# Kernel optimization log

Hardware: AMD Instinct MI355X
Metric: run time of the kernel (lower is better)

## Reference

```python
import jax, jax.numpy as jnp
import numpy as np

N_E = 512; KEY_DIM = 512; E_DIM = 512; E_SPLIT = 8
KT = 0.1; COE_EMA = 0.5; RATE = 1.2
HALF_PI = float(np.pi / 2.0)


def l2n(x, eps=1e-12):
    # torch F.normalize(p=2, dim=-1)
    return x / jnp.maximum(jnp.linalg.norm(x, axis=-1, keepdims=True), eps)


def sphere_emb(feature, t):
    # TimeSphereEncoder: lift unit feature in R^d to R^{d+1} with time angle
    # a = t * (pi/2) / rate ; out = [feature*cos(a), sin(a)]
    a = t * (HALF_PI / RATE)
    return jnp.concatenate([feature * jnp.cos(a)[..., None], jnp.sin(a)[..., None]], axis=-1)


def split_t_f(x):
    # inverse of sphere_emb for unit-norm x: recover (t, sin_component, feature)
    s = x[..., -1]
    t = jnp.arcsin(jnp.clip(s, -1.0, 1.0)) / (HALF_PI / RATE)
    f = l2n(x[..., :-1])
    return t, s, f


def split_norm(v):
    # split_vparams_norm: L2-normalize each of E_SPLIT contiguous chunks
    shp = v.shape
    d = E_DIM // E_SPLIT
    return l2n(v.reshape(shp[:-1] + (E_SPLIT, d))).reshape(shp)


def setup_inputs() -> dict:
    key = jax.random.key(0)
    k = jax.random.split(key, 6)
    key_soft = jax.random.normal(k[0], (32, 1024, KEY_DIM), jnp.float32)
    u_t = jax.random.uniform(k[1], (32, 1024), jnp.float32)
    keys_weight = l2n(jax.random.uniform(k[2], (N_E, KEY_DIM), jnp.float32, -1.0 / N_E, 1.0 / N_E))
    t_keys_weight = (jnp.arange(N_E, dtype=jnp.float32)[:, None]
                     + jax.random.uniform(k[3], (N_E, 1), jnp.float32)) / N_E
    r_keys_weight = jnp.full((N_E, 1), 0.999, jnp.float32)
    vparams_weight = jax.random.uniform(k[4], (N_E, E_DIM), jnp.float32, -1.0 / N_E, 1.0 / N_E)
    return {"key_soft": key_soft, "u_t": u_t, "keys_weight": keys_weight,
            "t_keys_weight": t_keys_weight, "r_keys_weight": r_keys_weight,
            "vparams_weight": vparams_weight}


def _forward(key_soft, u_t, keys_weight, t_keys_weight, r_keys_weight, vparams_weight):
    sg = jax.lax.stop_gradient
    B, T, D = key_soft.shape
    BT = B * T
    # normalize + time-embed tokens
    ks_emb = sphere_emb(l2n(key_soft), u_t)                       # (B,T,D+1)
    ks_flat = ks_emb.reshape(BT, D + 1)
    # codebook keys: normalized, time-embedded, detached, scaled by hardtanh(r)
    keys_norm = sphere_emb(l2n(keys_weight), t_keys_weight[:, 0])  # (n_e,D+1)
    r = jnp.clip(r_keys_weight, 0.0, 1.0)                          # (n_e,1)
    keysA = sg(keys_norm) * r
    score0 = ks_flat @ keysA.T                                     # (BT,n_e)
    idx0 = jnp.argmax(score0, axis=1)
    # --- EMA codebook update (all no-grad) ---
    ks_sg = sg(ks_flat)
    seg = jax.ops.segment_sum(ks_sg, idx0, num_segments=N_E)       # (n_e,D+1)
    cnt = jax.ops.segment_sum(jnp.ones((BT,), ks_sg.dtype), idx0, num_segments=N_E)[:, None]
    mean_ks = jnp.nan_to_num(seg / (1.0 + cnt))
    keys_new_full = l2n(sg(keysA) * COE_EMA + mean_ks * (1.0 - COE_EMA))
    t_new, _, feat_new = split_t_f(keys_new_full)
    index_switch = jnp.argsort(t_new)
    t_sorted = t_new[index_switch]
    keys_feat2 = feat_new[index_switch]
    r2 = jnp.clip(r_keys_weight[index_switch], 0.0, 1.0)
    vparams2 = vparams_weight[index_switch]
    idx1 = index_switch[idx0]
    cnt2 = jax.ops.segment_sum(jnp.ones((BT,), ks_sg.dtype), idx1, num_segments=N_E) + 1.0
    w_cnt = sg(jnp.nan_to_num(1.0 / cnt2)[idx1].reshape(B, T))
    # --- second scoring with updated codebook ---
    keys_norm2 = sphere_emb(l2n(keys_feat2), t_sorted)             # (n_e,D+1)
    keysB = sg(keys_norm2) * r2
    score = ks_flat @ keysB.T                                      # (BT,n_e)
    w = jnp.nan_to_num(jax.nn.softmax(score / KT, axis=-1))
    w_max = jnp.take_along_axis(w, idx1[:, None], axis=-1)[:, 0].reshape(B, T)
    vpn = split_norm(vparams2)
    vp_w = split_norm(w @ sg(vpn))                                 # (BT,e_dim)
    key_w = l2n(w @ sg(keysB))                                     # (BT,D+1)
    vparams_hard = split_norm(vparams2[idx1])
    key_hard_raw = keysB[idx1]
    vparams_hard = vp_w + sg(vparams_hard - vp_w)                  # straight-through
    key_hard = key_w + sg(key_hard_raw - key_w)
    return (idx1.reshape(B, T),
            key_hard.reshape(B, T, D + 1),
            vp_w.reshape(B, T, E_DIM),
            vparams_hard.reshape(B, T, E_DIM),
            w_max, w_cnt, ks_emb)


def reference(key_soft, u_t, keys_weight, t_keys_weight, r_keys_weight, vparams_weight):
    return _forward(key_soft, u_t, keys_weight, t_keys_weight, r_keys_weight, vparams_weight)
```

## Files before the change

### kernel.cpp

```cpp
#include <hip/hip_runtime.h>
#include <math.h>

constexpr int BT  = 32768;
constexpr int D   = 512;
constexpr int D1  = 513;
constexpr int NE  = 512;
constexpr int EDIM = 512;
constexpr int NCH = 128;
constexpr int SUB = 16;
constexpr int P1S = 520;
constexpr int AKP = 544;
#define KA 1.3089969389957472f

typedef _Float16 h16;
typedef _Float16 f16x8 __attribute__((ext_vector_type(8)));
typedef _Float16 f16x4 __attribute__((ext_vector_type(4)));
typedef float f32x4 __attribute__((ext_vector_type(4)));

__device__ __forceinline__ float wave_sum(float v) {
#pragma unroll
  for (int off = 32; off; off >>= 1) v += __shfl_xor(v, off);
  return v;
}

__global__ __launch_bounds__(256) void k_embed(const float* __restrict__ ks,
                                               const float* __restrict__ ut,
                                               float* __restrict__ emb) {
  int token = blockIdx.x * 4 + (threadIdx.x >> 6);
  int lane = threadIdx.x & 63;
  const float4* row4 = (const float4*)(ks + (size_t)token * D);
  float4 va = row4[lane * 2];
  float4 vb = row4[lane * 2 + 1];
  float ss = va.x * va.x + va.y * va.y + va.z * va.z + va.w * va.w
           + vb.x * vb.x + vb.y * vb.y + vb.z * vb.z + vb.w * vb.w;
  ss = wave_sum(ss);
  float inv = 1.0f / fmaxf(sqrtf(ss), 1e-12f);
  float a = ut[token] * KA;
  float c = cosf(a), s = sinf(a);
  float ic = inv * c;
  float* o = emb + (size_t)token * D1 + lane * 8;
  o[0] = va.x * ic; o[1] = va.y * ic; o[2] = va.z * ic; o[3] = va.w * ic;
  o[4] = vb.x * ic; o[5] = vb.y * ic; o[6] = vb.z * ic; o[7] = vb.w * ic;
  if (lane == 0) emb[(size_t)token * D1 + D] = s;
}

__global__ __launch_bounds__(64) void k_keysA(const float* __restrict__ kw,
                                              const float* __restrict__ tk,
                                              const float* __restrict__ rk,
                                              float* __restrict__ keysA) {
  int e = blockIdx.x; int lane = threadIdx.x;
  const float* row = kw + (size_t)e * D;
  float v[8]; float ss = 0.f;
#pragma unroll
  for (int i = 0; i < 8; i++) { v[i] = row[lane + 64 * i]; ss += v[i] * v[i]; }
  ss = wave_sum(ss);
  float inv = 1.0f / fmaxf(sqrtf(ss), 1e-12f);
  float a = tk[e] * KA;
  float r = fminf(fmaxf(rk[e], 0.f), 1.f);
  float c = cosf(a) * r, s = sinf(a) * r;
  float* o = keysA + (size_t)e * D1;
#pragma unroll
  for (int i = 0; i < 8; i++) o[lane + 64 * i] = v[i] * inv * c;
  if (lane == 0) o[D] = s;
}

__global__ __launch_bounds__(64) void k_split2(const float* __restrict__ in,
                                               h16* __restrict__ out,
                                               int ncol, int kp) {
  int e = blockIdx.x; int lane = threadIdx.x;
  const float* r = in + (size_t)e * ncol;
  h16* o = out + (size_t)e * 2 * kp;
  for (int c = lane; c < kp; c += 64) {
    float x = (c < ncol) ? r[c] * 8.0f : 0.f;
    h16 h = (h16)x;
    o[c] = h;
    o[kp + c] = (h16)(x - (float)h);
  }
}

template <int KP, int EPI, int ASRC, int TERMS>
__global__ __launch_bounds__(256) void k_gemm3(const float* __restrict__ Af,
                                               const h16* __restrict__ Ai,
                                               const h16* __restrict__ Bp,
                                               float* __restrict__ C,
                                               unsigned short* __restrict__ W,
                                               float* __restrict__ pv,
                                               int* __restrict__ pi_,
                                               float* __restrict__ ps) {
  constexpr int NS = KP / 32;
  constexpr int LST = 36;
  __shared__ h16 Ah[128 * LST];
  __shared__ h16 Al[(TERMS >= 2) ? 128 * LST : 1];
  __shared__ h16 Bh[128 * LST];
  __shared__ h16 Bl[(TERMS >= 3) ? 128 * LST : 1];
  const int tid = threadIdx.x;
  const int bid = blockIdx.x;
  const int wg = (bid & 7) * (gridDim.x >> 3) + (bid >> 3);
  const int m0 = (wg >> 2) * 128;
  const int n0 = (wg & 3) * 128;
  const int nblk = wg & 3;
  const int lane = tid & 63;
  const int wid = tid >> 6;
  const int wr = wid >> 1, wc = wid & 1;
  const int l15 = lane & 15, l4 = lane >> 4;
  const int aB = (wr * 64 + l15) * LST + l4 * 8;
  const int bB = (wc * 64 + l15) * LST + l4 * 8;

  f32x4 acc[4][4] = {};

  auto loadAf = [&](int s, float fv[4][4]) {
    int k0 = s * 32;
    bool guard = (KP == AKP) && (k0 + 32 > D1);
#pragma unroll
    for (int p = 0; p < 4; ++p) {
      int row = (tid >> 3) + 32 * p;
      int fq = tid & 7;
      const float* ap = Af + (size_t)(m0 + row) * D1 + k0 + fq * 4;
      if (!guard) {
#pragma unroll
        for (int j = 0; j < 4; ++j) fv[p][j] = ap[j];
      } else {
#pragma unroll
        for (int j = 0; j < 4; ++j) {
          int c = k0 + fq * 4 + j;
          fv[p][j] = (c < D1) ? ap[j] : 0.f;
        }
      }
    }
  };
  auto writeAf = [&](float fv[4][4]) {
#pragma unroll
    for (int p = 0; p < 4; ++p) {
      int row = (tid >> 3) + 32 * p;
      int fq = tid & 7;
      f16x4 hh, ll;
#pragma unroll
      for (int j = 0; j < 4; ++j) {
        float x = fv[p][j] * 8.0f;
        h16 h = (h16)x;
        hh[j] = h;
        ll[j] = (h16)(x - (float)h);
      }
      *(f16x4*)&Ah[row * LST + fq * 4] = hh;
      if constexpr (TERMS >= 2) *(f16x4*)&Al[row * LST + fq * 4] = ll;
    }
  };
  auto loadAi = [&](int s, uint4 av[2]) {
    int k0 = s * 32;
#pragma unroll
    for (int p = 0; p < 2; ++p) {
      int lin = tid + 256 * p;
      int row = lin >> 2, q = lin & 3;
      av[p] = *(const uint4*)(Ai + (size_t)(m0 + row) * 512 + k0 + q * 8);
    }
  };
  auto writeAi = [&](uint4 av[2]) {
#pragma unroll
    for (int p = 0; p < 2; ++p) {
      int lin = tid + 256 * p;
      int row = lin >> 2, q = lin & 3;
      *(uint4*)&Ah[row * LST + q * 8] = av[p];
    }
  };
  constexpr int BPASS = (TERMS >= 3) ? 4 : 2;
  auto loadB = [&](int s, uint4 bv[BPASS]) {
    int k0 = s * 32;
#pragma unroll
    for (int p = 0; p < BPASS; ++p) {
      int lin = tid + 256 * p;
      int row = (lin >> 2) & 127;
      int half = lin >> 9;
      int q = lin & 3;
      bv[p] = *(const uint4*)(Bp + (size_t)(n0 + row) * (2 * KP) + half * KP + k0 + q * 8);
    }
  };
  auto writeB = [&](uint4 bv[BPASS]) {
#pragma unroll
    for (int p = 0; p < BPASS; ++p) {
      int lin = tid + 256 * p;
      int row = (lin >> 2) & 127;
      int half = lin >> 9;
      int q = lin & 3;
      h16* dst = (half && TERMS >= 3) ? Bl : Bh;
      *(uint4*)&dst[row * LST + q * 8] = bv[p];
    }
  };

  {
    uint4 bv[BPASS];
    loadB(0, bv);
    if constexpr (ASRC == 0) { float fv[4][4]; loadAf(0, fv); writeAf(fv); }
    else { uint4 av[2]; loadAi(0, av); writeAi(av); }
    writeB(bv);
  }
  __syncthreads();

  for (int s = 0; s < NS; ++s) {
    uint4 avn[2], bvn[BPASS]; float fvn[4][4];
    if (s + 1 < NS) {
      if constexpr (ASRC == 0) loadAf(s + 1, fvn);
      else loadAi(s + 1, avn);
      loadB(s + 1, bvn);
    }
    f16x8 ah[4], al_[4];
#pragma unroll
    for (int i = 0; i < 4; ++i) {
      ah[i] = *(const f16x8*)&Ah[aB + i * 16 * LST];
      if constexpr (TERMS >= 2) al_[i] = *(const f16x8*)&Al[aB + i * 16 * LST];
    }
#pragma unroll
    for (int j = 0; j < 4; ++j) {
      f16x8 bh_ = *(const f16x8*)&Bh[bB + j * 16 * LST];
      f16x8 bl_;
      if constexpr (TERMS >= 3) bl_ = *(const f16x8*)&Bl[bB + j * 16 * LST];
#pragma unroll
      for (int i = 0; i < 4; ++i) {
        acc[i][j] = __builtin_amdgcn_mfma_f32_16x16x32_f16(ah[i], bh_, acc[i][j], 0, 0, 0);
        if constexpr (TERMS >= 2)
          acc[i][j] = __builtin_amdgcn_mfma_f32_16x16x32_f16(al_[i], bh_, acc[i][j], 0, 0, 0);
        if constexpr (TERMS >= 3)
          acc[i][j] = __builtin_amdgcn_mfma_f32_16x16x32_f16(ah[i], bl_, acc[i][j], 0, 0, 0);
      }
    }
    __syncthreads();
    if (s + 1 < NS) {
      if constexpr (ASRC == 0) writeAf(fvn);
      else writeAi(avn);
      writeB(bvn);
    }
    __syncthreads();
  }

  if constexpr (EPI == 1) {
#pragma unroll
    for (int i = 0; i < 4; ++i)
#pragma unroll
      for (int r = 0; r < 4; ++r) {
        float ss = 0.f;
#pragma unroll
        for (int j = 0; j < 4; ++j) ss += acc[i][j][r] * acc[i][j][r];
        ss += __shfl_xor(ss, 1); ss += __shfl_xor(ss, 2);
        ss += __shfl_xor(ss, 4); ss += __shfl_xor(ss, 8);
        float inv = 1.0f / fmaxf(sqrtf(ss), 1e-12f);
        int row = m0 + wr * 64 + i * 16 + l4 * 4 + r;
        float* cp = C + (size_t)row * 512 + n0 + wc * 64 + l15;
#pragma unroll
        for (int j = 0; j < 4; ++j) cp[j * 16] = acc[i][j][r] * inv;
      }
  } else if constexpr (EPI == 2) {
    float* lv = (float*)Ah;
    int*   li = (int*)Bh;
#pragma unroll
    for (int i = 0; i < 4; ++i)
#pragma unroll
      for (int r = 0; r < 4; ++r) {
        float bv = -INFINITY; int bidx = 0x7fffffff;
#pragma unroll
        for (int j = 0; j < 4; ++j) {
          float val = acc[i][j][r] * 0.015625f;
          int col = n0 + wc * 64 + j * 16 + l15;
          if (val > bv || (val == bv && col < bidx)) { bv = val; bidx = col; }
        }
#pragma unroll
        for (int off = 1; off < 16; off <<= 1) {
          float ov = __shfl_xor(bv, off);
          int oi = __shfl_xor(bidx, off);
          if (ov > bv || (ov == bv && oi < bidx)) { bv = ov; bidx = oi; }
        }
        if (l15 == 0) {
          int lr = wr * 64 + i * 16 + l4 * 4 + r;
          lv[wc * 128 + lr] = bv; li[wc * 128 + lr] = bidx;
        }
      }
    __syncthreads();
    if (tid < 128) {
      float v0 = lv[tid], v1 = lv[128 + tid];
      int i0 = li[tid], i1 = li[128 + tid];
      bool sec = (v1 > v0) || (v1 == v0 && i1 < i0);
      int row = m0 + tid;
      pv[(size_t)row * 4 + nblk] = sec ? v1 : v0;
      pi_[(size_t)row * 4 + nblk] = sec ? i1 : i0;
    }
  } else if constexpr (EPI == 3) {
    float* psW = (float*)Bh;
#pragma unroll
    for (int i = 0; i < 4; ++i)
#pragma unroll
      for (int r = 0; r < 4; ++r) {
        int row = m0 + wr * 64 + i * 16 + l4 * 4 + r;
        unsigned short* wp = W + (size_t)row * 512 + n0 + wc * 64 + l15;
        float se = 0.f;
#pragma unroll
        for (int j = 0; j < 4; ++j) {
          float v = acc[i][j][r] * 0.015625f;
          float w = __expf(10.f * v);
          se += w;
          h16 hh = (h16)w;
          wp[j * 16] = *(unsigned short*)&hh;
        }
        se += __shfl_xor(se, 1); se += __shfl_xor(se, 2);
        se += __shfl_xor(se, 4); se += __shfl_xor(se, 8);
        if (l15 == 0) psW[wc * 128 + wr * 64 + i * 16 + l4 * 4 + r] = se;
      }
    __syncthreads();
    if (tid < 128)
      ps[(size_t)(m0 + tid) * 4 + nblk] = psW[tid] + psW[128 + tid];
  }
}

__global__ __launch_bounds__(256) void k_argmax_fin(const float* __restrict__ pval,
                                                    const int* __restrict__ pidx,
                                                    int* __restrict__ idx0) {
  int t = blockIdx.x * 256 + threadIdx.x;
  float bv = pval[(size_t)t * 4];
  int bi = pidx[(size_t)t * 4];
#pragma unroll
  for (int b = 1; b < 4; ++b) {
    float v = pval[(size_t)t * 4 + b];
    if (v > bv) { bv = v; bi = pidx[(size_t)t * 4 + b]; }
  }
  idx0[t] = bi;
}

__global__ __launch_bounds__(256) void k_smfin(const float* __restrict__ ps,
                                               const unsigned short* __restrict__ W,
                                               const int* __restrict__ idx1,
                                               float* __restrict__ O4) {
  int t = blockIdx.x * 256 + threadIdx.x;
  float S = ps[(size_t)t * 4] + ps[(size_t)t * 4 + 1]
          + ps[(size_t)t * 4 + 2] + ps[(size_t)t * 4 + 3];
  unsigned short u = W[(size_t)t * 512 + idx1[t]];
  float wsel = (float)(*(const h16*)&u);
  O4[t] = wsel / S;
}

__global__ __launch_bounds__(256) void k_hist_chunks(const int* __restrict__ idx0,
                                                     int* __restrict__ hist2,
                                                     int* __restrict__ myrank) {
  __shared__ int lidx[256];
  __shared__ int hist[NE];
  int tid = threadIdx.x;
  int chunk = blockIdx.x;
  int t = chunk * 256 + tid;
  lidx[tid] = idx0[t];
  hist[tid] = 0; hist[tid + 256] = 0;
  __syncthreads();
  int j = lidx[tid];
  int rank = 0;
  for (int i = 0; i < tid; ++i) rank += (lidx[i] == j);
  myrank[t] = rank;
  atomicAdd(&hist[j], 1);
  __syncthreads();
  hist2[chunk * NE + tid] = hist[tid];
  hist2[chunk * NE + tid + 256] = hist[tid + 256];
}

__global__ __launch_bounds__(512) void k_scan(const int* __restrict__ hist2,
                                              int* __restrict__ offs,
                                              int* __restrict__ chunk_base,
                                              float* __restrict__ cntf) {
  __shared__ int sh[NE];
  int c = threadIdx.x;
  int tot = 0;
  for (int k = 0; k < NCH; ++k) tot += hist2[k * NE + c];
  cntf[c] = (float)tot;
  sh[c] = tot;
  __syncthreads();
  for (int off = 1; off < NE; off <<= 1) {
    int v = (c >= off) ? sh[c - off] : 0;
    __syncthreads();
    sh[c] += v;
    __syncthreads();
  }
  int excl = sh[c] - tot;
  offs[c] = excl;
  int run = excl;
  for (int k = 0; k < NCH; ++k) {
    chunk_base[k * NE + c] = run;
    run += hist2[k * NE + c];
  }
}

__global__ __launch_bounds__(256) void k_scatter(const int* __restrict__ idx0,
                                                 const int* __restrict__ myrank,
                                                 const int* __restrict__ chunk_base,
                                                 int* __restrict__ tok_sorted) {
  int tid = threadIdx.x;
  int chunk = blockIdx.x;
  int t = chunk * 256 + tid;
  int j = idx0[t];
  tok_sorted[chunk_base[chunk * NE + j] + myrank[t]] = t;
}

__global__ __launch_bounds__(256) void k_seg1(const int* __restrict__ tok_sorted,
                                              const int* __restrict__ offs,
                                              const float* __restrict__ cntf,
                                              const float* __restrict__ emb,
                                              float* __restrict__ part1) {
  __shared__ float part[4][512];
  __shared__ float p512[4];
  int e = blockIdx.x, sub = blockIdx.y;
  int tid = threadIdx.x;
  int wave = tid >> 6, lane = tid & 63;
  int start = offs[e];
  int n = (int)cntf[e];
  float acc[8] = {}; float a512 = 0.f;
  for (int k = sub * 4 + wave; k < n; k += SUB * 4) {
    int t = tok_sorted[start + k];
    const float* row = emb + (size_t)t * D1;
#pragma unroll
    for (int i = 0; i < 8; ++i) acc[i] += row[lane + 64 * i];
    if (lane == 0) a512 += row[512];
  }
#pragma unroll
  for (int i = 0; i < 8; ++i) part[wave][lane + 64 * i] = acc[i];
  if (lane == 0) p512[wave] = a512;
  __syncthreads();
  float* o = part1 + (size_t)(e * SUB + sub) * P1S;
  o[tid] = part[0][tid] + part[1][tid] + part[2][tid] + part[3][tid];
  o[tid + 256] = part[0][tid + 256] + part[1][tid + 256] + part[2][tid + 256] + part[3][tid + 256];
  if (tid == 0) o[512] = p512[0] + p512[1] + p512[2] + p512[3];
}

__global__ __launch_bounds__(256) void k_seg2(const float* __restrict__ part1,
                                              const float* __restrict__ cntf,
                                              const float* __restrict__ keysA,
                                              float* __restrict__ feat,
                                              float* __restrict__ tnew) {
  __shared__ float r4[4];
  __shared__ float r4b[4];
  int e = blockIdx.x;
  int tid = threadIdx.x;
  int wave = tid >> 6, lane = tid & 63;
  float s0 = 0.f, s1 = 0.f, s512 = 0.f;
  for (int sub = 0; sub < SUB; ++sub) {
    const float* p = part1 + (size_t)(e * SUB + sub) * P1S;
    s0 += p[tid]; s1 += p[tid + 256]; s512 += p[512];
  }
  float c = cntf[e];
  float rinv = 1.0f / (1.0f + c);
  float x0 = keysA[(size_t)e * D1 + tid] * 0.5f + (s0 * rinv) * 0.5f;
  float x1 = keysA[(size_t)e * D1 + tid + 256] * 0.5f + (s1 * rinv) * 0.5f;
  float x512 = keysA[(size_t)e * D1 + 512] * 0.5f + (s512 * rinv) * 0.5f;
  float ssp = x0 * x0 + x1 * x1;
  float w = wave_sum(ssp);
  if (lane == 0) r4[wave] = w;
  __syncthreads();
  float ss = r4[0] + r4[1] + r4[2] + r4[3] + x512 * x512;
  float inv = 1.0f / fmaxf(sqrtf(ss), 1e-12f);
  if (tid == 0) {
    float sc = fminf(fmaxf(x512 * inv, -1.0f), 1.0f);
    tnew[e] = asinf(sc) / KA;
  }
  float f0 = x0 * inv, f1 = x1 * inv;
  float ssp2 = f0 * f0 + f1 * f1;
  float w2 = wave_sum(ssp2);
  if (lane == 0) r4b[wave] = w2;
  __syncthreads();
  float ss2 = r4b[0] + r4b[1] + r4b[2] + r4b[3];
  float inv2 = 1.0f / fmaxf(sqrtf(ss2), 1e-12f);
  feat[(size_t)e * D + tid] = f0 * inv2;
  feat[(size_t)e * D + tid + 256] = f1 * inv2;
}

__global__ __launch_bounds__(512) void k_argsort(const float* __restrict__ tnew,
                                                 int* __restrict__ perm) {
  __shared__ float t[NE];
  int i = threadIdx.x;
  t[i] = tnew[i];
  __syncthreads();
  float ti = t[i];
  int rank = 0;
  for (int j = 0; j < NE; j++) {
    float tj = t[j];
    rank += (tj < ti) || (tj == ti && j < i);
  }
  perm[rank] = i;
}

__global__ __launch_bounds__(64) void k_build(const int* __restrict__ perm,
                                              const float* __restrict__ tnew,
                                              const float* __restrict__ rk,
                                              const float* __restrict__ feat,
                                              const float* __restrict__ vparams,
                                              float* __restrict__ keysB,
                                              float* __restrict__ vpn,
                                              h16* __restrict__ BV) {
  int p = blockIdx.x; int lane = threadIdx.x;
  int src = perm[p];
  float t = tnew[src];
  float a = t * KA;
  float r2 = fminf(fmaxf(rk[src], 0.f), 1.f);
  float f[8]; float ss = 0.f;
#pragma unroll
  for (int i = 0; i < 8; i++) { f[i] = feat[(size_t)src * D + lane + 64 * i]; ss += f[i] * f[i]; }
  ss = wave_sum(ss);
  float inv = 1.0f / fmaxf(sqrtf(ss), 1e-12f);
  float c = cosf(a) * r2, s = sinf(a) * r2;
#pragma unroll
  for (int i = 0; i < 8; i++) keysB[(size_t)p * D1 + lane + 64 * i] = f[i] * inv * c;
  if (lane == 0) keysB[(size_t)p * D1 + D] = s;
#pragma unroll
  for (int i = 0; i < 8; i++) {
    float vp = vparams[(size_t)src * EDIM + lane + 64 * i];
    float ssc = wave_sum(vp * vp);
    float invc = 1.0f / fmaxf(sqrtf(ssc), 1e-12f);
    float val = vp * invc;
    int d = lane + 64 * i;
    vpn[(size_t)p * EDIM + d] = val;
    float x = val * 8.0f;
    h16 hi = (h16)x;
    BV[(size_t)d * (2 * NE) + p] = hi;
    BV[(size_t)d * (2 * NE) + NE + p] = (h16)(x - (float)hi);
  }
}

__global__ __launch_bounds__(256) void k_idx1(const int* __restrict__ idx0,
                                              const int* __restrict__ perm,
                                              int* __restrict__ idx1,
                                              float* __restrict__ O0) {
  int t = blockIdx.x * 256 + threadIdx.x;
  int j = perm[idx0[t]];
  idx1[t] = j;
  O0[t] = (float)j;
}

__global__ __launch_bounds__(256) void k_gather(const int* __restrict__ idx1,
                                                const int* __restrict__ perm,
                                                const float* __restrict__ cntf,
                                                const float* __restrict__ keysB,
                                                const float* __restrict__ vpn,
                                                float* __restrict__ O1,
                                                float* __restrict__ O3,
                                                float* __restrict__ O5) {
  int t = blockIdx.x * 4 + (threadIdx.x >> 6);
  int lane = threadIdx.x & 63;
  int j = idx1[t];
#pragma unroll
  for (int i = 0; i < 9; i++) {
    int d = lane + 64 * i;
    if (d < D1) O1[(size_t)t * D1 + d] = keysB[(size_t)j * D1 + d];
  }
#pragma unroll
  for (int i = 0; i < 8; i++) {
    int d = lane + 64 * i;
    O3[(size_t)t * EDIM + d] = vpn[(size_t)j * EDIM + d];
  }
  if (lane == 0) O5[t] = 1.0f / (cntf[perm[j]] + 1.0f);
}

extern "C" void kernel_launch(void* const* d_in, const int* in_sizes, int n_in,
                              void* d_out, int out_size, void* d_ws, size_t ws_size,
                              hipStream_t stream) {
  const float* key_soft = (const float*)d_in[0];
  const float* u_t      = (const float*)d_in[1];
  const float* keys_w   = (const float*)d_in[2];
  const float* t_keys   = (const float*)d_in[3];
  const float* r_keys   = (const float*)d_in[4];
  const float* vparams  = (const float*)d_in[5];

  float* out = (float*)d_out;
  float* O0 = out;
  float* O1 = O0 + (size_t)BT;
  float* O2 = O1 + (size_t)BT * D1;
  float* O3 = O2 + (size_t)BT * EDIM;
  float* O4 = O3 + (size_t)BT * EDIM;
  float* O5 = O4 + (size_t)BT;
  float* O6 = O5 + (size_t)BT;

  float* ws = (float*)d_ws;
  size_t off = 0;
  auto alloc = [&](size_t n) { float* p = ws + off; off += (n + 63) & ~(size_t)63; return p; };
  unsigned short* w16 = (unsigned short*)alloc((size_t)BT * 256);
  float* part1  = alloc((size_t)NE * SUB * P1S);
  float* keysA  = alloc((size_t)NE * D1);
  float* keysB  = alloc((size_t)NE * D1);
  float* feat   = alloc((size_t)NE * D);
  float* vpn    = alloc((size_t)NE * EDIM);
  float* tnew   = alloc(NE);
  float* cntf   = alloc(NE);
  h16*   BA     = (h16*)alloc((size_t)NE * AKP);
  h16*   BB     = (h16*)alloc((size_t)NE * AKP);
  h16*   BV     = (h16*)alloc((size_t)EDIM * NE);
  float* pval   = alloc((size_t)BT * 4);
  int*   pidx   = (int*)alloc((size_t)BT * 4);
  float* ps2    = alloc((size_t)BT * 4);
  int*   idx0   = (int*)alloc(BT);
  int*   idx1   = (int*)alloc(BT);
  int*   perm   = (int*)alloc(NE);
  int*   myrank = (int*)alloc(BT);
  int*   tok_sorted = (int*)alloc(BT);
  int*   hist2  = (int*)alloc((size_t)NCH * NE);
  int*   chunk_base = (int*)alloc((size_t)NCH * NE);
  int*   offsb  = (int*)alloc(NE);

  k_embed<<<BT / 4, 256, 0, stream>>>(key_soft, u_t, O6);
  k_keysA<<<NE, 64, 0, stream>>>(keys_w, t_keys, r_keys, keysA);
  k_split2<<<NE, 64, 0, stream>>>(keysA, BA, D1, AKP);
  k_gemm3<AKP, 2, 0, 3><<<1024, 256, 0, stream>>>(O6, nullptr, BA,
                                                  nullptr, nullptr, pval, pidx, nullptr);
  k_argmax_fin<<<BT / 256, 256, 0, stream>>>(pval, pidx, idx0);
  k_hist_chunks<<<NCH, 256, 0, stream>>>(idx0, hist2, myrank);
  k_scan<<<1, NE, 0, stream>>>(hist2, offsb, chunk_base, cntf);
  k_scatter<<<NCH, 256, 0, stream>>>(idx0, myrank, chunk_base, tok_sorted);
  k_seg1<<<dim3(NE, SUB), 256, 0, stream>>>(tok_sorted, offsb, cntf, O6, part1);
  k_seg2<<<NE, 256, 0, stream>>>(part1, cntf, keysA, feat, tnew);
  k_argsort<<<1, NE, 0, stream>>>(tnew, perm);
  k_build<<<NE, 64, 0, stream>>>(perm, tnew, r_keys, feat, vparams, keysB, vpn, BV);
  k_split2<<<NE, 64, 0, stream>>>(keysB, BB, D1, AKP);
  k_idx1<<<BT / 256, 256, 0, stream>>>(idx0, perm, idx1, O0);
  k_gemm3<AKP, 3, 0, 2><<<1024, 256, 0, stream>>>(O6, nullptr, BB,
                                                  nullptr, w16, nullptr, nullptr, ps2);
  k_smfin<<<BT / 256, 256, 0, stream>>>(ps2, w16, idx1, O4);
  k_gemm3<512, 1, 2, 1><<<1024, 256, 0, stream>>>(nullptr, (const h16*)w16, BV,
                                                  O2, nullptr, nullptr, nullptr, nullptr);
  k_gather<<<BT / 4, 256, 0, stream>>>(idx1, perm, cntf, keysB, vpn, O1, O3, O5);
}
```

Before: 443.8 us.

## Precompute fp16 hi/lo split of token embeddings once and fuse small kernels

The embed kernel now also writes a padded fp16 hi/lo split of each token embedding. Both scoring GEMMs load this pre-split A directly instead of re-reading fp32 and splitting it in every tile. The codebook split is folded into k_keysA and k_build, and the argmax-finalize and idx1 kernels are merged into neighbouring kernels, which removes several launches. The cost is an extra 32768x1088 fp16 buffer written once and read twice, and k_seg1 now runs with SUB raised to 32.

```diff
diff --git a/kernel.cpp b/kernel.cpp
--- a/kernel.cpp
+++ b/kernel.cpp
@@ -7,9 +7,10 @@
 constexpr int NE  = 512;
 constexpr int EDIM = 512;
 constexpr int NCH = 128;
-constexpr int SUB = 16;
+constexpr int SUB = 32;
 constexpr int P1S = 520;
 constexpr int AKP = 544;
+constexpr int A16S = 2 * AKP;
 #define KA 1.3089969389957472f
 
 typedef _Float16 h16;
@@ -23,9 +24,20 @@
   return v;
 }
 
+__device__ __forceinline__ void split8(const float* v, float scale, f16x8& hh, f16x8& ll) {
+#pragma unroll
+  for (int j = 0; j < 8; ++j) {
+    float x = v[j] * scale;
+    h16 h = (h16)x;
+    hh[j] = h;
+    ll[j] = (h16)(x - (float)h);
+  }
+}
+
 __global__ __launch_bounds__(256) void k_embed(const float* __restrict__ ks,
                                                const float* __restrict__ ut,
-                                               float* __restrict__ emb) {
+                                               float* __restrict__ emb,
+                                               h16* __restrict__ A16) {
   int token = blockIdx.x * 4 + (threadIdx.x >> 6);
   int lane = threadIdx.x & 63;
   const float4* row4 = (const float4*)(ks + (size_t)token * D);
@@ -38,16 +50,35 @@
   float a = ut[token] * KA;
   float c = cosf(a), s = sinf(a);
   float ic = inv * c;
+  float vals[8] = {va.x * ic, va.y * ic, va.z * ic, va.w * ic,
+                   vb.x * ic, vb.y * ic, vb.z * ic, vb.w * ic};
   float* o = emb + (size_t)token * D1 + lane * 8;
-  o[0] = va.x * ic; o[1] = va.y * ic; o[2] = va.z * ic; o[3] = va.w * ic;
-  o[4] = vb.x * ic; o[5] = vb.y * ic; o[6] = vb.z * ic; o[7] = vb.w * ic;
-  if (lane == 0) emb[(size_t)token * D1 + D] = s;
+#pragma unroll
+  for (int j = 0; j < 8; ++j) o[j] = vals[j];
+  h16* ar = A16 + (size_t)token * A16S;
+  f16x8 hh, ll;
+  split8(vals, 8.0f, hh, ll);
+  *(f16x8*)&ar[lane * 8] = hh;
+  *(f16x8*)&ar[AKP + lane * 8] = ll;
+  if (lane < 4) {
+    f16x8 th = {}, tl = {};
+    if (lane == 0) {
+      emb[(size_t)token * D1 + D] = s;
+      float x = s * 8.0f;
+      h16 h = (h16)x;
+      th[0] = h;
+      tl[0] = (h16)(x - (float)h);
+    }
+    *(f16x8*)&ar[512 + lane * 8] = th;
+    *(f16x8*)&ar[AKP + 512 + lane * 8] = tl;
+  }
 }
 
 __global__ __launch_bounds__(64) void k_keysA(const float* __restrict__ kw,
                                               const float* __restrict__ tk,
                                               const float* __restrict__ rk,
-                                              float* __restrict__ keysA) {
+                                              float* __restrict__ keysA,
+                                              h16* __restrict__ BA) {
   int e = blockIdx.x; int lane = threadIdx.x;
   const float* row = kw + (size_t)e * D;
   float v[8]; float ss = 0.f;
@@ -59,28 +90,31 @@
   float r = fminf(fmaxf(rk[e], 0.f), 1.f);
   float c = cosf(a) * r, s = sinf(a) * r;
   float* o = keysA + (size_t)e * D1;
-#pragma unroll
-  for (int i = 0; i < 8; i++) o[lane + 64 * i] = v[i] * inv * c;
-  if (lane == 0) o[D] = s;
-}
-
-__global__ __launch_bounds__(64) void k_split2(const float* __restrict__ in,
-                                               h16* __restrict__ out,
-                                               int ncol, int kp) {
-  int e = blockIdx.x; int lane = threadIdx.x;
-  const float* r = in + (size_t)e * ncol;
-  h16* o = out + (size_t)e * 2 * kp;
-  for (int c = lane; c < kp; c += 64) {
-    float x = (c < ncol) ? r[c] * 8.0f : 0.f;
+  h16* br = BA + (size_t)e * A16S;
+#pragma unroll
+  for (int i = 0; i < 8; i++) {
+    float val = v[i] * inv * c;
+    o[lane + 64 * i] = val;
+    float x = val * 8.0f;
     h16 h = (h16)x;
-    o[c] = h;
-    o[kp + c] = (h16)(x - (float)h);
+    br[lane + 64 * i] = h;
+    br[AKP + lane + 64 * i] = (h16)(x - (float)h);
+  }
+  if (lane == 0) {
+    o[D] = s;
+    float x = s * 8.0f;
+    h16 h = (h16)x;
+    br[512] = h;
+    br[AKP + 512] = (h16)(x - (float)h);
+  }
+  if (lane >= 1 && lane < 32) {
+    br[512 + lane] = (h16)0.f;
+    br[AKP + 512 + lane] = (h16)0.f;
   }
 }
 
 template <int KP, int EPI, int ASRC, int TERMS>
-__global__ __launch_bounds__(256) void k_gemm3(const float* __restrict__ Af,
-                                               const h16* __restrict__ Ai,
+__global__ __launch_bounds__(256) void k_gemm4(const h16* __restrict__ Ai,
                                                const h16* __restrict__ Bp,
                                                float* __restrict__ C,
                                                unsigned short* __restrict__ W,
@@ -108,44 +142,29 @@
 
   f32x4 acc[4][4] = {};
 
-  auto loadAf = [&](int s, float fv[4][4]) {
+  auto loadA16 = [&](int s, uint4 av[4]) {
     int k0 = s * 32;
-    bool guard = (KP == AKP) && (k0 + 32 > D1);
 #pragma unroll
     for (int p = 0; p < 4; ++p) {
-      int row = (tid >> 3) + 32 * p;
-      int fq = tid & 7;
-      const float* ap = Af + (size_t)(m0 + row) * D1 + k0 + fq * 4;
-      if (!guard) {
-#pragma unroll
-        for (int j = 0; j < 4; ++j) fv[p][j] = ap[j];
-      } else {
-#pragma unroll
-        for (int j = 0; j < 4; ++j) {
-          int c = k0 + fq * 4 + j;
-          fv[p][j] = (c < D1) ? ap[j] : 0.f;
-        }
-      }
+      int lin = tid + 256 * p;
+      int row = (lin >> 2) & 127;
+      int half = lin >> 9;
+      int q = lin & 3;
+      av[p] = *(const uint4*)(Ai + (size_t)(m0 + row) * (2 * KP) + half * KP + k0 + q * 8);
     }
   };
-  auto writeAf = [&](float fv[4][4]) {
+  auto writeA16 = [&](uint4 av[4]) {
 #pragma unroll
     for (int p = 0; p < 4; ++p) {
-      int row = (tid >> 3) + 32 * p;
-      int fq = tid & 7;
-      f16x4 hh, ll;
-#pragma unroll
-      for (int j = 0; j < 4; ++j) {
-        float x = fv[p][j] * 8.0f;
-        h16 h = (h16)x;
-        hh[j] = h;
-        ll[j] = (h16)(x - (float)h);
-      }
-      *(f16x4*)&Ah[row * LST + fq * 4] = hh;
-      if constexpr (TERMS >= 2) *(f16x4*)&Al[row * LST + fq * 4] = ll;
+      int lin = tid + 256 * p;
+      int row = (lin >> 2) & 127;
+      int half = lin >> 9;
+      int q = lin & 3;
+      h16* dst = (half && TERMS >= 2) ? Al : Ah;
+      *(uint4*)&dst[row * LST + q * 8] = av[p];
     }
   };
-  auto loadAi = [&](int s, uint4 av[2]) {
+  auto loadAp = [&](int s, uint4 av[2]) {
     int k0 = s * 32;
 #pragma unroll
     for (int p = 0; p < 2; ++p) {
@@ -154,7 +173,7 @@
       av[p] = *(const uint4*)(Ai + (size_t)(m0 + row) * 512 + k0 + q * 8);
     }
   };
-  auto writeAi = [&](uint4 av[2]) {
+  auto writeAp = [&](uint4 av[2]) {
 #pragma unroll
     for (int p = 0; p < 2; ++p) {
       int lin = tid + 256 * p;
@@ -189,17 +208,17 @@
   {
     uint4 bv[BPASS];
     loadB(0, bv);
-    if constexpr (ASRC == 0) { float fv[4][4]; loadAf(0, fv); writeAf(fv); }
-    else { uint4 av[2]; loadAi(0, av); writeAi(av); }
+    if constexpr (ASRC == 1) { uint4 av[4]; loadA16(0, av); writeA16(av); }
+    else { uint4 av[2]; loadAp(0, av); writeAp(av); }
     writeB(bv);
   }
   __syncthreads();
 
   for (int s = 0; s < NS; ++s) {
-    uint4 avn[2], bvn[BPASS]; float fvn[4][4];
+    uint4 avn[4], apn[2], bvn[BPASS];
     if (s + 1 < NS) {
-      if constexpr (ASRC == 0) loadAf(s + 1, fvn);
-      else loadAi(s + 1, avn);
+      if constexpr (ASRC == 1) loadA16(s + 1, avn);
+      else loadAp(s + 1, apn);
       loadB(s + 1, bvn);
     }
     f16x8 ah[4], al_[4];
@@ -224,8 +243,8 @@
     }
     __syncthreads();
     if (s + 1 < NS) {
-      if constexpr (ASRC == 0) writeAf(fvn);
-      else writeAi(avn);
+      if constexpr (ASRC == 1) writeA16(avn);
+      else writeAp(apn);
       writeB(bvn);
     }
     __syncthreads();
@@ -308,33 +327,9 @@
   }
 }
 
-__global__ __launch_bounds__(256) void k_argmax_fin(const float* __restrict__ pval,
-                                                    const int* __restrict__ pidx,
-                                                    int* __restrict__ idx0) {
-  int t = blockIdx.x * 256 + threadIdx.x;
-  float bv = pval[(size_t)t * 4];
-  int bi = pidx[(size_t)t * 4];
-#pragma unroll
-  for (int b = 1; b < 4; ++b) {
-    float v = pval[(size_t)t * 4 + b];
-    if (v > bv) { bv = v; bi = pidx[(size_t)t * 4 + b]; }
-  }
-  idx0[t] = bi;
-}
-
-__global__ __launch_bounds__(256) void k_smfin(const float* __restrict__ ps,
-                                               const unsigned short* __restrict__ W,
-                                               const int* __restrict__ idx1,
-                                               float* __restrict__ O4) {
-  int t = blockIdx.x * 256 + threadIdx.x;
-  float S = ps[(size_t)t * 4] + ps[(size_t)t * 4 + 1]
-          + ps[(size_t)t * 4 + 2] + ps[(size_t)t * 4 + 3];
-  unsigned short u = W[(size_t)t * 512 + idx1[t]];
-  float wsel = (float)(*(const h16*)&u);
-  O4[t] = wsel / S;
-}
-
-__global__ __launch_bounds__(256) void k_hist_chunks(const int* __restrict__ idx0,
+__global__ __launch_bounds__(256) void k_hist_chunks(const float* __restrict__ pval,
+                                                     const int* __restrict__ pidx,
+                                                     int* __restrict__ idx0,
                                                      int* __restrict__ hist2,
                                                      int* __restrict__ myrank) {
   __shared__ int lidx[256];
@@ -342,7 +337,15 @@
   int tid = threadIdx.x;
   int chunk = blockIdx.x;
   int t = chunk * 256 + tid;
-  lidx[tid] = idx0[t];
+  float bv = pval[(size_t)t * 4];
+  int bi = pidx[(size_t)t * 4];
+#pragma unroll
+  for (int b = 1; b < 4; ++b) {
+    float v = pval[(size_t)t * 4 + b];
+    if (v > bv) { bv = v; bi = pidx[(size_t)t * 4 + b]; }
+  }
+  idx0[t] = bi;
+  lidx[tid] = bi;
   hist[tid] = 0; hist[tid + 256] = 0;
   __syncthreads();
   int j = lidx[tid];
@@ -484,6 +487,7 @@
                                               const float* __restrict__ feat,
                                               const float* __restrict__ vparams,
                                               float* __restrict__ keysB,
+                                              h16* __restrict__ BB,
                                               float* __restrict__ vpn,
                                               h16* __restrict__ BV) {
   int p = blockIdx.x; int lane = threadIdx.x;
@@ -497,9 +501,27 @@
   ss = wave_sum(ss);
   float inv = 1.0f / fmaxf(sqrtf(ss), 1e-12f);
   float c = cosf(a) * r2, s = sinf(a) * r2;
-#pragma unroll
-  for (int i = 0; i < 8; i++) keysB[(size_t)p * D1 + lane + 64 * i] = f[i] * inv * c;
-  if (lane == 0) keysB[(size_t)p * D1 + D] = s;
+  h16* br = BB + (size_t)p * A16S;
+#pragma unroll
+  for (int i = 0; i < 8; i++) {
+    float val = f[i] * inv * c;
+    keysB[(size_t)p * D1 + lane + 64 * i] = val;
+    float x = val * 8.0f;
+    h16 h = (h16)x;
+    br[lane + 64 * i] = h;
+    br[AKP + lane + 64 * i] = (h16)(x - (float)h);
+  }
+  if (lane == 0) {
+    keysB[(size_t)p * D1 + D] = s;
+    float x = s * 8.0f;
+    h16 h = (h16)x;
+    br[512] = h;
+    br[AKP + 512] = (h16)(x - (float)h);
+  }
+  if (lane >= 1 && lane < 32) {
+    br[512 + lane] = (h16)0.f;
+    br[AKP + 512 + lane] = (h16)0.f;
+  }
 #pragma unroll
   for (int i = 0; i < 8; i++) {
     float vp = vparams[(size_t)src * EDIM + lane + 64 * i];
@@ -515,27 +537,33 @@
   }
 }
 
-__global__ __launch_bounds__(256) void k_idx1(const int* __restrict__ idx0,
-                                              const int* __restrict__ perm,
-                                              int* __restrict__ idx1,
-                                              float* __restrict__ O0) {
+__global__ __launch_bounds__(256) void k_smfin(const float* __restrict__ ps,
+                                               const unsigned short* __restrict__ W,
+                                               const int* __restrict__ perm,
+                                               const int* __restrict__ idx0,
+                                               float* __restrict__ O4) {
   int t = blockIdx.x * 256 + threadIdx.x;
+  float S = ps[(size_t)t * 4] + ps[(size_t)t * 4 + 1]
+          + ps[(size_t)t * 4 + 2] + ps[(size_t)t * 4 + 3];
   int j = perm[idx0[t]];
-  idx1[t] = j;
-  O0[t] = (float)j;
-}
-
-__global__ __launch_bounds__(256) void k_gather(const int* __restrict__ idx1,
+  unsigned short u = W[(size_t)t * 512 + j];
+  float wsel = (float)(*(const h16*)&u);
+  O4[t] = wsel / S;
+}
+
+__global__ __launch_bounds__(256) void k_gather(const int* __restrict__ idx0,
                                                 const int* __restrict__ perm,
                                                 const float* __restrict__ cntf,
                                                 const float* __restrict__ keysB,
                                                 const float* __restrict__ vpn,
+                                                float* __restrict__ O0,
                                                 float* __restrict__ O1,
                                                 float* __restrict__ O3,
                                                 float* __restrict__ O5) {
   int t = blockIdx.x * 4 + (threadIdx.x >> 6);
   int lane = threadIdx.x & 63;
-  int j = idx1[t];
+  int i0 = idx0[t];
+  int j = perm[i0];
 #pragma unroll
   for (int i = 0; i < 9; i++) {
     int d = lane + 64 * i;
@@ -546,7 +574,10 @@
     int d = lane + 64 * i;
     O3[(size_t)t * EDIM + d] = vpn[(size_t)j * EDIM + d];
   }
-  if (lane == 0) O5[t] = 1.0f / (cntf[perm[j]] + 1.0f);
+  if (lane == 0) {
+    O0[t] = (float)j;
+    O5[t] = 1.0f / (cntf[i0] + 1.0f);
+  }
 }
 
 extern "C" void kernel_launch(void* const* d_in, const int* in_sizes, int n_in,
@@ -572,6 +603,7 @@
   size_t off = 0;
   auto alloc = [&](size_t n) { float* p = ws + off; off += (n + 63) & ~(size_t)63; return p; };
   unsigned short* w16 = (unsigned short*)alloc((size_t)BT * 256);
+  h16*   A16    = (h16*)alloc((size_t)BT * AKP);
   float* part1  = alloc((size_t)NE * SUB * P1S);
   float* keysA  = alloc((size_t)NE * D1);
   float* keysB  = alloc((size_t)NE * D1);
@@ -586,7 +618,6 @@
   int*   pidx   = (int*)alloc((size_t)BT * 4);
   float* ps2    = alloc((size_t)BT * 4);
   int*   idx0   = (int*)alloc(BT);
-  int*   idx1   = (int*)alloc(BT);
   int*   perm   = (int*)alloc(NE);
   int*   myrank = (int*)alloc(BT);
   int*   tok_sorted = (int*)alloc(BT);
@@ -594,25 +625,21 @@
   int*   chunk_base = (int*)alloc((size_t)NCH * NE);
   int*   offsb  = (int*)alloc(NE);
 
-  k_embed<<<BT / 4, 256, 0, stream>>>(key_soft, u_t, O6);
-  k_keysA<<<NE, 64, 0, stream>>>(keys_w, t_keys, r_keys, keysA);
-  k_split2<<<NE, 64, 0, stream>>>(keysA, BA, D1, AKP);
-  k_gemm3<AKP, 2, 0, 3><<<1024, 256, 0, stream>>>(O6, nullptr, BA,
+  k_embed<<<BT / 4, 256, 0, stream>>>(key_soft, u_t, O6, A16);
+  k_keysA<<<NE, 64, 0, stream>>>(keys_w, t_keys, r_keys, keysA, BA);
+  k_gemm4<AKP, 2, 1, 3><<<1024, 256, 0, stream>>>(A16, BA,
                                                   nullptr, nullptr, pval, pidx, nullptr);
-  k_argmax_fin<<<BT / 256, 256, 0, stream>>>(pval, pidx, idx0);
-  k_hist_chunks<<<NCH, 256, 0, stream>>>(idx0, hist2, myrank);
+  k_hist_chunks<<<NCH, 256, 0, stream>>>(pval, pidx, idx0, hist2, myrank);
   k_scan<<<1, NE, 0, stream>>>(hist2, offsb, chunk_base, cntf);
   k_scatter<<<NCH, 256, 0, stream>>>(idx0, myrank, chunk_base, tok_sorted);
   k_seg1<<<dim3(NE, SUB), 256, 0, stream>>>(tok_sorted, offsb, cntf, O6, part1);
   k_seg2<<<NE, 256, 0, stream>>>(part1, cntf, keysA, feat, tnew);
   k_argsort<<<1, NE, 0, stream>>>(tnew, perm);
-  k_build<<<NE, 64, 0, stream>>>(perm, tnew, r_keys, feat, vparams, keysB, vpn, BV);
-  k_split2<<<NE, 64, 0, stream>>>(keysB, BB, D1, AKP);
-  k_idx1<<<BT / 256, 256, 0, stream>>>(idx0, perm, idx1, O0);
-  k_gemm3<AKP, 3, 0, 2><<<1024, 256, 0, stream>>>(O6, nullptr, BB,
+  k_build<<<NE, 64, 0, stream>>>(perm, tnew, r_keys, feat, vparams, keysB, BB, vpn, BV);
+  k_gemm4<AKP, 3, 1, 2><<<1024, 256, 0, stream>>>(A16, BB,
                                                   nullptr, w16, nullptr, nullptr, ps2);
-  k_smfin<<<BT / 256, 256, 0, stream>>>(ps2, w16, idx1, O4);
-  k_gemm3<512, 1, 2, 1><<<1024, 256, 0, stream>>>(nullptr, (const h16*)w16, BV,
+  k_smfin<<<BT / 256, 256, 0, stream>>>(ps2, w16, perm, idx0, O4);
+  k_gemm4<512, 1, 2, 1><<<1024, 256, 0, stream>>>((const h16*)w16, BV,
                                                   O2, nullptr, nullptr, nullptr, nullptr);
-  k_gather<<<BT / 4, 256, 0, stream>>>(idx1, perm, cntf, keysB, vpn, O1, O3, O5);
-}
+  k_gather<<<BT / 4, 256, 0, stream>>>(idx0, perm, cntf, keysB, vpn, O0, O1, O3, O5);
+}
```

Measured after the change: 561.0 us. +26.4%, slower.
